# Performance work log

Hardware: AMD Instinct MI355X
Metric: run time of the kernel (lower is better)

The kernel has to match this reference:

```python
import jax, jax.numpy as jnp
import numpy as np
from jax import lax

B, T, C = 64, 50000, 4
MSYN, D, PATCH = 4, 160, 25
K_ENV, K_BUR, K_PRE = 25, 9, 9
DN = ('NCW', 'OIW', 'NCW')


def _dwconv(x, w, pad):
    # depthwise conv1d, x: [B,C,T], w: [C,1,K]
    return lax.conv_general_dilated(x, w, (1,), [(pad, pad)],
                                    dimension_numbers=DN,
                                    feature_group_count=x.shape[1])


def setup_inputs() -> dict:
    key = jax.random.key(0)
    ks = jax.random.split(key, 8)
    X = jax.random.normal(ks[0], (B, T, C), dtype=jnp.float32)
    M = jnp.ones((B, T, C), dtype=jnp.float32)
    s = 0.1
    w_env = jax.random.normal(ks[1], (C, 1, K_ENV), dtype=jnp.float32) * s
    w_burst = jax.random.normal(ks[2], (C, 1, K_BUR), dtype=jnp.float32) * s
    synergy_raw = jax.random.normal(ks[3], (MSYN, C), dtype=jnp.float32) * s
    w_pre_dw = jax.random.normal(ks[4], (MSYN, 1, K_PRE), dtype=jnp.float32) * s
    w_pre_pw = jax.random.normal(ks[5], (MSYN, MSYN, 1), dtype=jnp.float32) * s
    w_proj = jax.random.normal(ks[6], (D, MSYN, PATCH), dtype=jnp.float32) * s
    ln_gamma = jnp.ones((D,), dtype=jnp.float32)
    ln_beta = jnp.zeros((D,), dtype=jnp.float32)
    return {"X": X, "M": M, "w_env": w_env, "w_burst": w_burst,
            "synergy_raw": synergy_raw, "w_pre_dw": w_pre_dw,
            "w_pre_pw": w_pre_pw, "w_proj": w_proj,
            "ln_gamma": ln_gamma, "ln_beta": ln_beta}


def reference(X, M, w_env, w_burst, synergy_raw, w_pre_dw, w_pre_pw, w_proj, ln_gamma, ln_beta):
    # x: [B,C,T]
    x = (X * M).transpose(0, 2, 1)
    env = _dwconv(jnp.abs(x), w_env, K_ENV // 2)
    dx = jnp.pad(x[:, :, 1:] - x[:, :, :-1], ((0, 0), (0, 0), (1, 0)))
    burst = _dwconv(jnp.abs(dx), w_burst, K_BUR // 2)
    xm = 0.9 * env + 0.6 * burst + 0.2 * x
    # row-normalized softplus synergy matrix [Msyn, C]
    W = jax.nn.softplus(synergy_raw)
    W = W / jnp.maximum(W.sum(axis=1, keepdims=True), 1e-6)
    S = jnp.einsum('mc,bct->bmt', W, xm)
    Mm = (M.transpose(0, 2, 1) > 0).astype(x.dtype)
    Sm = jnp.clip(jnp.einsum('mc,bct->bmt', W, Mm), 0.0, 1.0)
    # pre: depthwise conv k=9 -> GELU -> 1x1 conv -> GELU (dropout = identity in eval)
    S = jax.nn.gelu(_dwconv(S, w_pre_dw, K_PRE // 2), approximate=False)
    S = jax.nn.gelu(jnp.einsum('om,bmt->bot', w_pre_pw[:, :, 0], S), approximate=False)
    S = S.transpose(0, 2, 1)          # [B,T,Msyn]
    Sm = Sm.transpose(0, 2, 1)        # [B,T,Msyn]
    # PatchProject1D
    p = PATCH
    T2 = (S.shape[1] // p) * p
    S = S[:, :T2, :]
    Sm = Sm[:, :T2, :]
    xs = (S * Sm).transpose(0, 2, 1)  # [B,Msyn,T2]
    h = lax.conv_general_dilated(xs, w_proj, (p,), 'VALID',
                                 dimension_numbers=DN).transpose(0, 2, 1)  # [B,L,D]
    mu = h.mean(axis=-1, keepdims=True)
    var = ((h - mu) ** 2).mean(axis=-1, keepdims=True)
    h = (h - mu) * lax.rsqrt(var + 1e-5) * ln_gamma + ln_beta
    # patchify time mask
    m_time = (Sm.mean(axis=-1) > 0).astype(jnp.float32)       # [B,T2]
    L = T2 // p
    m_patch = (m_time.reshape(Sm.shape[0], L, p).mean(axis=-1) > 0.1).astype(jnp.float32)
    return (h, m_patch)
```

## Files before the change

### kernel.cpp

```cpp
#include <hip/hip_runtime.h>
#include <hip/hip_bf16.h>
#include <cstddef>

#define T_LEN 50000

typedef __attribute__((ext_vector_type(8))) short bf16x8;
typedef __attribute__((ext_vector_type(4))) float f32x4;

__device__ __forceinline__ float sp_(float x){ return (x > 20.f) ? x : log1pf(expf(x)); }
__device__ __forceinline__ float gelu1(float x){ return 0.5f*x*(1.f + erff(x*0.7071067811865475f)); }

__global__ void k_cvtw(const float* __restrict__ wproj, __hip_bfloat16* __restrict__ wbf)
{
    int idx = blockIdx.x*256 + threadIdx.x;
    if (idx < 160*128) {
        int d = idx >> 7, i = idx & 127;
        float v = (i < 100) ? wproj[d*100 + i] : 0.f;
        wbf[idx] = __float2bfloat16(v);
    }
}

__global__ __launch_bounds__(256) void k_pre(
    const float* __restrict__ X, const float* __restrict__ Mq,
    const float* __restrict__ w_env, const float* __restrict__ w_bur,
    const float* __restrict__ syn, const float* __restrict__ wdw,
    const float* __restrict__ wpw,
    __hip_bfloat16* __restrict__ xs_out, float* __restrict__ mpatch)
{
    __shared__ float4 xb[1290];
    __shared__ float4 s1b[1260];
    __shared__ unsigned char maskb[1032];
    __shared__ float WnL[16];
    __shared__ float4 SmLUT[16];
    __shared__ __align__(16) __hip_bfloat16 abf[40*128];
    __shared__ float mtL[1000];

    const int tid  = threadIdx.x;
    const int b    = blockIdx.x / 50;
    const int tile = blockIdx.x % 50;
    const int t0   = tile * 1000;

    const float4* X4 = (const float4*)X + (size_t)b * T_LEN;
    const float4* M4 = (const float4*)Mq + (size_t)b * T_LEN;
    #pragma unroll
    for (int jj = 0; jj < 5; ++jj) {
        int idx = tid + jj*256;
        if (idx < 1032) {
            int t = t0 - 16 + idx;
            float4 xv = make_float4(0.f,0.f,0.f,0.f);
            unsigned mk = 0u;
            if (t >= 0 && t < T_LEN) {
                float4 a = X4[t], m = M4[t];
                xv = make_float4(a.x*m.x, a.y*m.y, a.z*m.z, a.w*m.w);
                mk = (m.x>0.f?1u:0u) | (m.y>0.f?2u:0u) | (m.z>0.f?4u:0u) | (m.w>0.f?8u:0u);
            }
            xb[idx + (idx>>2)] = xv;
            maskb[idx] = (unsigned char)mk;
        }
    }
    for (int idx = tid; idx < 40*28; idx += 256) {
        int p = idx / 28, i = 100 + idx % 28;
        abf[p*128 + i] = __float2bfloat16(0.f);
    }
    if (tid < 4) {
        float w0 = sp_(syn[tid*4+0]), w1 = sp_(syn[tid*4+1]);
        float w2 = sp_(syn[tid*4+2]), w3 = sp_(syn[tid*4+3]);
        float inv = 1.f / fmaxf(w0+w1+w2+w3, 1e-6f);
        WnL[tid*4+0]=w0*inv; WnL[tid*4+1]=w1*inv; WnL[tid*4+2]=w2*inv; WnL[tid*4+3]=w3*inv;
    }
    __syncthreads();
    if (tid < 16) {
        float sm[4];
        #pragma unroll
        for (int m=0;m<4;++m) {
            float a = 0.f;
            #pragma unroll
            for (int c=0;c<4;++c) if (tid & (1<<c)) a += WnL[m*4+c];
            sm[m] = fminf(a, 1.f);
        }
        SmLUT[tid] = make_float4(sm[0],sm[1],sm[2],sm[3]);
    }

    if (tid < 252) {
        float4 env[4], bur[4], xk[4];
        #pragma unroll
        for (int j=0;j<4;++j){ env[j]=make_float4(0,0,0,0); bur[j]=make_float4(0,0,0,0); }
        float4 xprev = make_float4(0,0,0,0);
        const int base  = 4*tid;
        const int gbase = t0 - 4 + 4*tid;
        #pragma unroll
        for (int s = -12; s <= 15; ++s) {
            int lt = base + (s+12);
            float4 xc = xb[lt + (lt>>2)];
            float4 ax = make_float4(fabsf(xc.x),fabsf(xc.y),fabsf(xc.z),fabsf(xc.w));
            if (s >= -4 && s <= 7) {
                int g = gbase + s;
                float4 dx;
                if (g <= 0 || g >= T_LEN) dx = make_float4(0,0,0,0);
                else dx = make_float4(xc.x-xprev.x, xc.y-xprev.y, xc.z-xprev.z, xc.w-xprev.w);
                float4 adx = make_float4(fabsf(dx.x),fabsf(dx.y),fabsf(dx.z),fabsf(dx.w));
                #pragma unroll
                for (int j=0;j<4;++j) {
                    int bk = s + 4 - j;
                    if (bk >= 0 && bk < 9) {
                        float b0=w_bur[bk], b1=w_bur[9+bk], b2=w_bur[18+bk], b3=w_bur[27+bk];
                        bur[j].x = fmaf(b0, adx.x, bur[j].x);
                        bur[j].y = fmaf(b1, adx.y, bur[j].y);
                        bur[j].z = fmaf(b2, adx.z, bur[j].z);
                        bur[j].w = fmaf(b3, adx.w, bur[j].w);
                    }
                }
            }
            #pragma unroll
            for (int j=0;j<4;++j) {
                int k = s + 12 - j;
                if (k >= 0 && k < 25) {
                    float e0=w_env[k], e1=w_env[25+k], e2=w_env[50+k], e3=w_env[75+k];
                    env[j].x = fmaf(e0, ax.x, env[j].x);
                    env[j].y = fmaf(e1, ax.y, env[j].y);
                    env[j].z = fmaf(e2, ax.z, env[j].z);
                    env[j].w = fmaf(e3, ax.w, env[j].w);
                }
            }
            if (s >= 0 && s <= 3) xk[s] = xc;
            xprev = xc;
        }
        #pragma unroll
        for (int j=0;j<4;++j) {
            int g = gbase + j;
            float4 xm = make_float4(
                0.9f*env[j].x + 0.6f*bur[j].x + 0.2f*xk[j].x,
                0.9f*env[j].y + 0.6f*bur[j].y + 0.2f*xk[j].y,
                0.9f*env[j].z + 0.6f*bur[j].z + 0.2f*xk[j].z,
                0.9f*env[j].w + 0.6f*bur[j].w + 0.2f*xk[j].w);
            float4 out = make_float4(0,0,0,0);
            if (g >= 0 && g < T_LEN) {
                out.x = WnL[0]*xm.x  + WnL[1]*xm.y  + WnL[2]*xm.z  + WnL[3]*xm.w;
                out.y = WnL[4]*xm.x  + WnL[5]*xm.y  + WnL[6]*xm.z  + WnL[7]*xm.w;
                out.z = WnL[8]*xm.x  + WnL[9]*xm.y  + WnL[10]*xm.z + WnL[11]*xm.w;
                out.w = WnL[12]*xm.x + WnL[13]*xm.y + WnL[14]*xm.z + WnL[15]*xm.w;
            }
            int ls = base + j;
            s1b[ls + (ls>>2)] = out;
        }
    }
    __syncthreads();

    if (tid < 250) {
        float4 s2a[4];
        #pragma unroll
        for (int j=0;j<4;++j) s2a[j]=make_float4(0,0,0,0);
        const int base = 4*tid;
        #pragma unroll
        for (int s = -4; s <= 7; ++s) {
            int ls = base + s + 4;
            float4 sc = s1b[ls + (ls>>2)];
            #pragma unroll
            for (int j=0;j<4;++j) {
                int k = s + 4 - j;
                if (k >= 0 && k < 9) {
                    float d0=wdw[k], d1=wdw[9+k], d2=wdw[18+k], d3=wdw[27+k];
                    s2a[j].x = fmaf(d0, sc.x, s2a[j].x);
                    s2a[j].y = fmaf(d1, sc.y, s2a[j].y);
                    s2a[j].z = fmaf(d2, sc.z, s2a[j].z);
                    s2a[j].w = fmaf(d3, sc.w, s2a[j].w);
                }
            }
        }
        #pragma unroll
        for (int j=0;j<4;++j) {
            int t = base + j;
            float g0 = gelu1(s2a[j].x), g1 = gelu1(s2a[j].y);
            float g2 = gelu1(s2a[j].z), g3 = gelu1(s2a[j].w);
            float4 sm = SmLUT[maskb[t + 16]];
            int p = t / 25, k = t % 25;
            float smv[4] = {sm.x, sm.y, sm.z, sm.w};
            #pragma unroll
            for (int o=0;o<4;++o) {
                float v = wpw[o*4+0]*g0 + wpw[o*4+1]*g1 + wpw[o*4+2]*g2 + wpw[o*4+3]*g3;
                abf[p*128 + o*25 + k] = __float2bfloat16(gelu1(v) * smv[o]);
            }
            mtL[t] = sm.x + sm.y + sm.z + sm.w;
        }
    }
    __syncthreads();

    {
        const float4* src = (const float4*)abf;
        float4* dst = (float4*)(xs_out + (size_t)(b*2000 + tile*40)*128);
        #pragma unroll
        for (int it = 0; it < 3; ++it) {
            int idx = tid + it*256;
            if (idx < 640) dst[idx] = src[idx];
        }
    }
    if (tid < 40) {
        int cnt = 0;
        #pragma unroll
        for (int k=0;k<25;++k) cnt += (mtL[tid*25+k] > 0.f) ? 1 : 0;
        mpatch[(size_t)b*2000 + tile*40 + tid] = (cnt >= 3) ? 1.f : 0.f;
    }
}

__global__ __launch_bounds__(256) void k_proj(
    const __hip_bfloat16* __restrict__ wbf, const __hip_bfloat16* __restrict__ xsg,
    const float* __restrict__ gamma, const float* __restrict__ beta,
    float* __restrict__ hout)
{
    __shared__ __align__(16) unsigned short Wl[160*136];
    __shared__ __align__(16) unsigned short Al[64*136];
    const int tid  = threadIdx.x;
    const int wv   = tid >> 6, lane = tid & 63;
    const int n    = lane & 15, quad = lane >> 4;

    {
        const float4* wg = (const float4*)wbf;
        #pragma unroll
        for (int it = 0; it < 10; ++it) {
            int idx = tid + it*256;
            int row = idx >> 4, cir = idx & 15;
            *(float4*)(Wl + row*136 + cir*8) = wg[idx];
        }
    }
    float gm[10], bt_[10];
    #pragma unroll
    for (int t = 0; t < 10; ++t) { gm[t] = gamma[t*16 + n]; bt_[t] = beta[t*16 + n]; }

    for (int bt = 0; bt < 2; ++bt) {
        const int p0 = (blockIdx.x*2 + bt) * 64;
        __syncthreads();
        {
            const float4* ag = (const float4*)(xsg + (size_t)p0*128);
            #pragma unroll
            for (int it = 0; it < 4; ++it) {
                int idx = tid + it*256;
                int row = idx >> 4, cir = idx & 15;
                *(float4*)(Al + row*136 + cir*8) = ag[idx];
            }
        }
        __syncthreads();

        f32x4 acc[10];
        #pragma unroll
        for (int t = 0; t < 10; ++t) acc[t] = (f32x4){0.f,0.f,0.f,0.f};
        #pragma unroll
        for (int kk = 0; kk < 4; ++kk) {
            bf16x8 af = *(const bf16x8*)(Al + (wv*16 + n)*136 + kk*32 + quad*8);
            #pragma unroll
            for (int t = 0; t < 10; ++t) {
                bf16x8 bf = *(const bf16x8*)(Wl + (t*16 + n)*136 + kk*32 + quad*8);
                acc[t] = __builtin_amdgcn_mfma_f32_16x16x32_bf16(af, bf, acc[t], 0, 0, 0);
            }
        }

        float mu[4], rs[4];
        #pragma unroll
        for (int r = 0; r < 4; ++r) {
            float a = 0.f;
            #pragma unroll
            for (int t = 0; t < 10; ++t) a += acc[t][r];
            a += __shfl_xor(a, 1, 64); a += __shfl_xor(a, 2, 64);
            a += __shfl_xor(a, 4, 64); a += __shfl_xor(a, 8, 64);
            mu[r] = a * (1.f/160.f);
        }
        #pragma unroll
        for (int r = 0; r < 4; ++r) {
            float q = 0.f;
            #pragma unroll
            for (int t = 0; t < 10; ++t) { float dv = acc[t][r] - mu[r]; q = fmaf(dv, dv, q); }
            q += __shfl_xor(q, 1, 64); q += __shfl_xor(q, 2, 64);
            q += __shfl_xor(q, 4, 64); q += __shfl_xor(q, 8, 64);
            rs[r] = rsqrtf(q * (1.f/160.f) + 1e-5f);
        }
        const int prow = p0 + wv*16 + quad*4;
        #pragma unroll
        for (int t = 0; t < 10; ++t) {
            #pragma unroll
            for (int r = 0; r < 4; ++r) {
                hout[(size_t)(prow + r)*160 + t*16 + n] = (acc[t][r] - mu[r])*rs[r]*gm[t] + bt_[t];
            }
        }
    }
}

extern "C" void kernel_launch(void* const* d_in, const int* in_sizes, int n_in,
                              void* d_out, int out_size, void* d_ws, size_t ws_size,
                              hipStream_t stream) {
    const float* X     = (const float*)d_in[0];
    const float* M     = (const float*)d_in[1];
    const float* w_env = (const float*)d_in[2];
    const float* w_bur = (const float*)d_in[3];
    const float* syn   = (const float*)d_in[4];
    const float* wdw   = (const float*)d_in[5];
    const float* wpw   = (const float*)d_in[6];
    const float* wproj = (const float*)d_in[7];
    const float* gam   = (const float*)d_in[8];
    const float* bet   = (const float*)d_in[9];

    float* h      = (float*)d_out;
    float* mpatch = h + (size_t)64*2000*160;

    __hip_bfloat16* wbf = (__hip_bfloat16*)d_ws;
    __hip_bfloat16* xsb = (__hip_bfloat16*)((char*)d_ws + 65536);

    k_cvtw<<<80, 256, 0, stream>>>(wproj, wbf);
    k_pre<<<3200, 256, 0, stream>>>(X, M, w_env, w_bur, syn, wdw, wpw, xsb, mpatch);
    k_proj<<<1000, 256, 0, stream>>>(wbf, xsb, gam, bet, h);
}
```

Baseline: 256.6 us.

## Halve pre-kernel tile, alias shared buffers, and drop LDS staging in projection

The preprocessing kernel now handles 500 timesteps per block instead of 1000, computes 2 outputs per thread instead of 4, and places all its shared arrays in one aliased buffer so the output staging reuses the input region. Together with a launch-bounds hint, this cuts shared memory and register use so more blocks can stay resident. The projection kernel no longer stages weights and activations in LDS: each wave loads its A fragment and the bf16 weights straight from global memory, one 16-row tile per wave, with no block barriers. The trade-offs are more halo recomputation per output in the pre kernel and repeated weight reads from global/L2 in the projection kernel.

Result: slower. 537.3 us (+109.4%).

```diff
diff --git a/kernel.cpp b/kernel.cpp
--- a/kernel.cpp
+++ b/kernel.cpp
@@ -20,32 +20,33 @@
     }
 }
 
-__global__ __launch_bounds__(256) void k_pre(
+__global__ __launch_bounds__(256, 5) void k_pre(
     const float* __restrict__ X, const float* __restrict__ Mq,
     const float* __restrict__ w_env, const float* __restrict__ w_bur,
     const float* __restrict__ syn, const float* __restrict__ wdw,
     const float* __restrict__ wpw,
     __hip_bfloat16* __restrict__ xs_out, float* __restrict__ mpatch)
 {
-    __shared__ float4 xb[1290];
-    __shared__ float4 s1b[1260];
-    __shared__ unsigned char maskb[1032];
-    __shared__ float WnL[16];
-    __shared__ float4 SmLUT[16];
-    __shared__ __align__(16) __hip_bfloat16 abf[40*128];
-    __shared__ float mtL[1000];
+    __shared__ __align__(16) char smem[21664];
+    float4* xb            = (float4*)smem;
+    float4* s1b           = (float4*)(smem + 10640);
+    unsigned char* maskb  = (unsigned char*)(smem + 20800);
+    float* WnL            = (float*)(smem + 21344);
+    float4* SmLUT         = (float4*)(smem + 21408);
+    __hip_bfloat16* abf   = (__hip_bfloat16*)smem;
+    float* mtL            = (float*)(smem + 5120);
 
     const int tid  = threadIdx.x;
-    const int b    = blockIdx.x / 50;
-    const int tile = blockIdx.x % 50;
-    const int t0   = tile * 1000;
+    const int b    = blockIdx.x / 100;
+    const int tile = blockIdx.x % 100;
+    const int t0   = tile * 500;
 
     const float4* X4 = (const float4*)X + (size_t)b * T_LEN;
     const float4* M4 = (const float4*)Mq + (size_t)b * T_LEN;
     #pragma unroll
-    for (int jj = 0; jj < 5; ++jj) {
+    for (int jj = 0; jj < 3; ++jj) {
         int idx = tid + jj*256;
-        if (idx < 1032) {
+        if (idx < 532) {
             int t = t0 - 16 + idx;
             float4 xv = make_float4(0.f,0.f,0.f,0.f);
             unsigned mk = 0u;
@@ -58,10 +59,6 @@
             maskb[idx] = (unsigned char)mk;
         }
     }
-    for (int idx = tid; idx < 40*28; idx += 256) {
-        int p = idx / 28, i = 100 + idx % 28;
-        abf[p*128 + i] = __float2bfloat16(0.f);
-    }
     if (tid < 4) {
         float w0 = sp_(syn[tid*4+0]), w1 = sp_(syn[tid*4+1]);
         float w2 = sp_(syn[tid*4+2]), w3 = sp_(syn[tid*4+3]);
@@ -80,27 +77,28 @@
         }
         SmLUT[tid] = make_float4(sm[0],sm[1],sm[2],sm[3]);
     }
-
-    if (tid < 252) {
-        float4 env[4], bur[4], xk[4];
-        #pragma unroll
-        for (int j=0;j<4;++j){ env[j]=make_float4(0,0,0,0); bur[j]=make_float4(0,0,0,0); }
+    __syncthreads();
+
+    if (tid < 254) {
+        float4 env[2], bur[2], xk[2];
+        #pragma unroll
+        for (int j=0;j<2;++j){ env[j]=make_float4(0,0,0,0); bur[j]=make_float4(0,0,0,0); }
         float4 xprev = make_float4(0,0,0,0);
-        const int base  = 4*tid;
-        const int gbase = t0 - 4 + 4*tid;
-        #pragma unroll
-        for (int s = -12; s <= 15; ++s) {
+        const int base  = 2*tid;
+        const int gbase = t0 - 4 + base;
+        #pragma unroll
+        for (int s = -12; s <= 13; ++s) {
             int lt = base + (s+12);
             float4 xc = xb[lt + (lt>>2)];
             float4 ax = make_float4(fabsf(xc.x),fabsf(xc.y),fabsf(xc.z),fabsf(xc.w));
-            if (s >= -4 && s <= 7) {
+            if (s >= -4 && s <= 5) {
                 int g = gbase + s;
                 float4 dx;
                 if (g <= 0 || g >= T_LEN) dx = make_float4(0,0,0,0);
                 else dx = make_float4(xc.x-xprev.x, xc.y-xprev.y, xc.z-xprev.z, xc.w-xprev.w);
                 float4 adx = make_float4(fabsf(dx.x),fabsf(dx.y),fabsf(dx.z),fabsf(dx.w));
                 #pragma unroll
-                for (int j=0;j<4;++j) {
+                for (int j=0;j<2;++j) {
                     int bk = s + 4 - j;
                     if (bk >= 0 && bk < 9) {
                         float b0=w_bur[bk], b1=w_bur[9+bk], b2=w_bur[18+bk], b3=w_bur[27+bk];
@@ -112,7 +110,7 @@
                 }
             }
             #pragma unroll
-            for (int j=0;j<4;++j) {
+            for (int j=0;j<2;++j) {
                 int k = s + 12 - j;
                 if (k >= 0 && k < 25) {
                     float e0=w_env[k], e1=w_env[25+k], e2=w_env[50+k], e3=w_env[75+k];
@@ -122,11 +120,11 @@
                     env[j].w = fmaf(e3, ax.w, env[j].w);
                 }
             }
-            if (s >= 0 && s <= 3) xk[s] = xc;
+            if (s >= 0 && s <= 1) xk[s] = xc;
             xprev = xc;
         }
         #pragma unroll
-        for (int j=0;j<4;++j) {
+        for (int j=0;j<2;++j) {
             int g = gbase + j;
             float4 xm = make_float4(
                 0.9f*env[j].x + 0.6f*bur[j].x + 0.2f*xk[j].x,
@@ -146,17 +144,21 @@
     }
     __syncthreads();
 
+    for (int idx = tid; idx < 20*28; idx += 256) {
+        int p = idx / 28, i = 100 + idx % 28;
+        abf[p*128 + i] = __float2bfloat16(0.f);
+    }
     if (tid < 250) {
-        float4 s2a[4];
-        #pragma unroll
-        for (int j=0;j<4;++j) s2a[j]=make_float4(0,0,0,0);
-        const int base = 4*tid;
-        #pragma unroll
-        for (int s = -4; s <= 7; ++s) {
+        float4 s2a[2];
+        #pragma unroll
+        for (int j=0;j<2;++j) s2a[j]=make_float4(0,0,0,0);
+        const int base = 2*tid;
+        #pragma unroll
+        for (int s = -4; s <= 5; ++s) {
             int ls = base + s + 4;
             float4 sc = s1b[ls + (ls>>2)];
             #pragma unroll
-            for (int j=0;j<4;++j) {
+            for (int j=0;j<2;++j) {
                 int k = s + 4 - j;
                 if (k >= 0 && k < 9) {
                     float d0=wdw[k], d1=wdw[9+k], d2=wdw[18+k], d3=wdw[27+k];
@@ -168,7 +170,7 @@
             }
         }
         #pragma unroll
-        for (int j=0;j<4;++j) {
+        for (int j=0;j<2;++j) {
             int t = base + j;
             float g0 = gelu1(s2a[j].x), g1 = gelu1(s2a[j].y);
             float g2 = gelu1(s2a[j].z), g3 = gelu1(s2a[j].w);
@@ -187,98 +189,80 @@
 
     {
         const float4* src = (const float4*)abf;
-        float4* dst = (float4*)(xs_out + (size_t)(b*2000 + tile*40)*128);
-        #pragma unroll
-        for (int it = 0; it < 3; ++it) {
+        float4* dst = (float4*)(xs_out + (size_t)(b*2000 + tile*20)*128);
+        #pragma unroll
+        for (int it = 0; it < 2; ++it) {
             int idx = tid + it*256;
-            if (idx < 640) dst[idx] = src[idx];
-        }
-    }
-    if (tid < 40) {
+            if (idx < 320) dst[idx] = src[idx];
+        }
+    }
+    if (tid < 20) {
         int cnt = 0;
         #pragma unroll
         for (int k=0;k<25;++k) cnt += (mtL[tid*25+k] > 0.f) ? 1 : 0;
-        mpatch[(size_t)b*2000 + tile*40 + tid] = (cnt >= 3) ? 1.f : 0.f;
-    }
-}
-
-__global__ __launch_bounds__(256) void k_proj(
+        mpatch[(size_t)b*2000 + tile*20 + tid] = (cnt >= 3) ? 1.f : 0.f;
+    }
+}
+
+__global__ __launch_bounds__(256, 4) void k_proj(
     const __hip_bfloat16* __restrict__ wbf, const __hip_bfloat16* __restrict__ xsg,
     const float* __restrict__ gamma, const float* __restrict__ beta,
     float* __restrict__ hout)
 {
-    __shared__ __align__(16) unsigned short Wl[160*136];
-    __shared__ __align__(16) unsigned short Al[64*136];
     const int tid  = threadIdx.x;
     const int wv   = tid >> 6, lane = tid & 63;
     const int n    = lane & 15, quad = lane >> 4;
-
-    {
-        const float4* wg = (const float4*)wbf;
-        #pragma unroll
-        for (int it = 0; it < 10; ++it) {
-            int idx = tid + it*256;
-            int row = idx >> 4, cir = idx & 15;
-            *(float4*)(Wl + row*136 + cir*8) = wg[idx];
-        }
-    }
+    const int p0   = (blockIdx.x*4 + wv) * 16;
+
+    const unsigned short* Wp = (const unsigned short*)wbf;
+    const unsigned short* Ap = (const unsigned short*)xsg;
+
+    bf16x8 af[4];
+    #pragma unroll
+    for (int kk=0;kk<4;++kk)
+        af[kk] = *(const bf16x8*)(Ap + (size_t)(p0 + n)*128 + kk*32 + quad*8);
+
     float gm[10], bt_[10];
     #pragma unroll
     for (int t = 0; t < 10; ++t) { gm[t] = gamma[t*16 + n]; bt_[t] = beta[t*16 + n]; }
 
-    for (int bt = 0; bt < 2; ++bt) {
-        const int p0 = (blockIdx.x*2 + bt) * 64;
-        __syncthreads();
-        {
-            const float4* ag = (const float4*)(xsg + (size_t)p0*128);
-            #pragma unroll
-            for (int it = 0; it < 4; ++it) {
-                int idx = tid + it*256;
-                int row = idx >> 4, cir = idx & 15;
-                *(float4*)(Al + row*136 + cir*8) = ag[idx];
-            }
-        }
-        __syncthreads();
-
-        f32x4 acc[10];
-        #pragma unroll
-        for (int t = 0; t < 10; ++t) acc[t] = (f32x4){0.f,0.f,0.f,0.f};
-        #pragma unroll
-        for (int kk = 0; kk < 4; ++kk) {
-            bf16x8 af = *(const bf16x8*)(Al + (wv*16 + n)*136 + kk*32 + quad*8);
-            #pragma unroll
-            for (int t = 0; t < 10; ++t) {
-                bf16x8 bf = *(const bf16x8*)(Wl + (t*16 + n)*136 + kk*32 + quad*8);
-                acc[t] = __builtin_amdgcn_mfma_f32_16x16x32_bf16(af, bf, acc[t], 0, 0, 0);
-            }
-        }
-
-        float mu[4], rs[4];
+    f32x4 acc[10];
+    #pragma unroll
+    for (int t = 0; t < 10; ++t) acc[t] = (f32x4){0.f,0.f,0.f,0.f};
+    #pragma unroll
+    for (int kk = 0; kk < 4; ++kk) {
+        #pragma unroll
+        for (int t = 0; t < 10; ++t) {
+            bf16x8 bf = *(const bf16x8*)(Wp + (size_t)(t*16 + n)*128 + kk*32 + quad*8);
+            acc[t] = __builtin_amdgcn_mfma_f32_16x16x32_bf16(af[kk], bf, acc[t], 0, 0, 0);
+        }
+    }
+
+    float mu[4], rs[4];
+    #pragma unroll
+    for (int r = 0; r < 4; ++r) {
+        float a = 0.f;
+        #pragma unroll
+        for (int t = 0; t < 10; ++t) a += acc[t][r];
+        a += __shfl_xor(a, 1, 64); a += __shfl_xor(a, 2, 64);
+        a += __shfl_xor(a, 4, 64); a += __shfl_xor(a, 8, 64);
+        mu[r] = a * (1.f/160.f);
+    }
+    #pragma unroll
+    for (int r = 0; r < 4; ++r) {
+        float q = 0.f;
+        #pragma unroll
+        for (int t = 0; t < 10; ++t) { float dv = acc[t][r] - mu[r]; q = fmaf(dv, dv, q); }
+        q += __shfl_xor(q, 1, 64); q += __shfl_xor(q, 2, 64);
+        q += __shfl_xor(q, 4, 64); q += __shfl_xor(q, 8, 64);
+        rs[r] = rsqrtf(q * (1.f/160.f) + 1e-5f);
+    }
+    const int prow = p0 + quad*4;
+    #pragma unroll
+    for (int t = 0; t < 10; ++t) {
         #pragma unroll
         for (int r = 0; r < 4; ++r) {
-            float a = 0.f;
-            #pragma unroll
-            for (int t = 0; t < 10; ++t) a += acc[t][r];
-            a += __shfl_xor(a, 1, 64); a += __shfl_xor(a, 2, 64);
-            a += __shfl_xor(a, 4, 64); a += __shfl_xor(a, 8, 64);
-            mu[r] = a * (1.f/160.f);
-        }
-        #pragma unroll
-        for (int r = 0; r < 4; ++r) {
-            float q = 0.f;
-            #pragma unroll
-            for (int t = 0; t < 10; ++t) { float dv = acc[t][r] - mu[r]; q = fmaf(dv, dv, q); }
-            q += __shfl_xor(q, 1, 64); q += __shfl_xor(q, 2, 64);
-            q += __shfl_xor(q, 4, 64); q += __shfl_xor(q, 8, 64);
-            rs[r] = rsqrtf(q * (1.f/160.f) + 1e-5f);
-        }
-        const int prow = p0 + wv*16 + quad*4;
-        #pragma unroll
-        for (int t = 0; t < 10; ++t) {
-            #pragma unroll
-            for (int r = 0; r < 4; ++r) {
-                hout[(size_t)(prow + r)*160 + t*16 + n] = (acc[t][r] - mu[r])*rs[r]*gm[t] + bt_[t];
-            }
+            hout[(size_t)(prow + r)*160 + t*16 + n] = (acc[t][r] - mu[r])*rs[r]*gm[t] + bt_[t];
         }
     }
 }
@@ -304,6 +288,6 @@
     __hip_bfloat16* xsb = (__hip_bfloat16*)((char*)d_ws + 65536);
 
     k_cvtw<<<80, 256, 0, stream>>>(wproj, wbf);
-    k_pre<<<3200, 256, 0, stream>>>(X, M, w_env, w_bur, syn, wdw, wpw, xsb, mpatch);
-    k_proj<<<1000, 256, 0, stream>>>(wbf, xsb, gam, bet, h);
-}
+    k_pre<<<6400, 256, 0, stream>>>(X, M, w_env, w_bur, syn, wdw, wpw, xsb, mpatch);
+    k_proj<<<2000, 256, 0, stream>>>(wbf, xsb, gam, bet, h);
+}
```
